# Kernel tuning notes

Hardware: AMD Instinct MI355X
Metric: run time of the kernel (lower is better)

The kernel has to match this reference:

```python
import jax, jax.numpy as jnp
import numpy as np

B, A, N_IN, N_POINTS = 64, 256, 512, 2048


def _sq_cdist(u, v):
    # |u_i - v_j|^2 via expansion, abs() as in the torch original
    d = -2.0 * (u @ v.T) + (u * u).sum(1)[:, None] + (v * v).sum(1)[None, :]
    return jnp.abs(d)


def setup_inputs() -> dict:
    key = jax.random.key(0)
    k1, k2, k3, k4 = jax.random.split(key, 4)
    x = jax.random.normal(k1, (B, A, N_IN), dtype=jnp.float32)
    atom_mask = jax.random.bernoulli(k2, 0.8, (B, A))  # ragged valid-atom mask
    inducing_points = jax.random.normal(k3, (N_POINTS, N_IN), dtype=jnp.float32)
    gamma = (1.0 + 0.25 * jax.random.normal(k4, (N_IN,), dtype=jnp.float32)) * np.sqrt(N_IN).astype(np.float32)
    return {"x": x, "atom_mask": atom_mask, "inducing_points": inducing_points, "gamma": gamma}


def reference(x, atom_mask, inducing_points, gamma):
    b, a, n_in = x.shape
    m = atom_mask.astype(x.dtype)                      # [B, A]
    mf = m[..., None]                                  # [B, A, 1]
    n = m.sum()
    # masked mean / unbiased std over valid atoms (torch .std is ddof=1)
    mean = (x * mf).sum((0, 1)) / n                    # [n_in]
    var = (((x - mean) ** 2) * mf).sum((0, 1)) / (n - 1.0)
    std = jnp.sqrt(var) + 1e-5                         # [n_in]
    xn = (x - mean) / std * mf                         # zero out padded atoms

    g2 = gamma ** 2 + 0.001                            # [n_in]
    z = (xn / g2).reshape(b * a, n_in)                 # [N, n_in]
    zi = inducing_points / g2                          # [M, n_in]

    Kx = jnp.exp(-_sq_cdist(z, zi))                    # [N, M]
    Kind = jnp.exp(-_sq_cdist(zi, zi))                 # [M, M]
    Kinv = jnp.linalg.inv(Kind + 0.05 * jnp.eye(Kind.shape[0], dtype=x.dtype))

    t = Kx @ Kinv                                      # [N, M]
    x_new = ((t @ inducing_points) * std + mean).reshape(b, a, n_in) * mf
    var_out = (1.0 - (t * Kx).sum(-1)).reshape(b, a) * m
    return x_new, var_out
```

## Files before the change

### kernel.cpp

```cpp
#include <hip/hip_runtime.h>
#include <math.h>
#include <stdint.h>

namespace {

constexpr int NROW = 16384;
constexpr int NF   = 512;
constexpr int MIND = 2048;
constexpr float CC = 0.98f;

typedef _Float16 half8 __attribute__((ext_vector_type(8)));
typedef float floatx4 __attribute__((ext_vector_type(4)));

__device__ __forceinline__ void gload16(const void* g, void* l) {
  __builtin_amdgcn_global_load_lds(
      (__attribute__((address_space(1))) void*)g,
      (__attribute__((address_space(3))) void*)l, 16, 0, 0);
}

__global__ __launch_bounds__(256) void stats_kernel(
    const float* __restrict__ x, const int* __restrict__ mask,
    float* __restrict__ sum, float* __restrict__ sumsq, float* __restrict__ cnt)
{
  const int t = threadIdx.x;
  const int row0 = blockIdx.x * 64;
  float s0 = 0.f, s1 = 0.f, q0 = 0.f, q1 = 0.f, c = 0.f;
  for (int r = 0; r < 64; ++r) {
    const int row = row0 + r;
    const float m = (mask[row] != 0) ? 1.f : 0.f;
    const float v0 = x[(size_t)row * NF + t];
    const float v1 = x[(size_t)row * NF + t + 256];
    s0 += m * v0; q0 += m * v0 * v0;
    s1 += m * v1; q1 += m * v1 * v1;
    c += m;
  }
  atomicAdd(&sum[t], s0);        atomicAdd(&sum[t + 256], s1);
  atomicAdd(&sumsq[t], q0);      atomicAdd(&sumsq[t + 256], q1);
  if (t == 0) atomicAdd(cnt, c);
}

__global__ __launch_bounds__(256) void finalize_stats(
    const float* __restrict__ sum, const float* __restrict__ sumsq,
    const float* __restrict__ cnt, const float* __restrict__ gamma,
    float* __restrict__ meanv, float* __restrict__ stdv,
    float* __restrict__ zsv, float* __restrict__ giv)
{
  const int f = blockIdx.x * 256 + threadIdx.x;
  const float n = cnt[0];
  const float mu = sum[f] / n;
  const float var = (sumsq[f] - sum[f] * mu) / (n - 1.0f);
  const float sd = sqrtf(var) + 1e-5f;
  const float g = gamma[f];
  const float g2 = g * g + 0.001f;
  meanv[f] = mu;
  stdv[f]  = sd;
  zsv[f]   = 1.0f / (sd * g2);
  giv[f]   = 1.0f / g2;
}

__global__ __launch_bounds__(256) void make_z(
    const float* __restrict__ x, const int* __restrict__ mask,
    const float* __restrict__ ip, const float* __restrict__ meanv,
    const float* __restrict__ zsv, const float* __restrict__ giv,
    _Float16* __restrict__ Zh, _Float16* __restrict__ Zih,
    float* __restrict__ rnorm, float* __restrict__ cnorm)
{
  const int row = blockIdx.x;
  const int t = threadIdx.x;
  float v0, v1;
  if (row < NROW) {
    const float m = (mask[row] != 0) ? 1.f : 0.f;
    v0 = (x[(size_t)row * NF + t      ] - meanv[t      ]) * zsv[t      ] * m;
    v1 = (x[(size_t)row * NF + t + 256] - meanv[t + 256]) * zsv[t + 256] * m;
    const _Float16 h0 = (_Float16)v0, h1 = (_Float16)v1;
    Zh[(size_t)row * NF + t] = h0;
    Zh[(size_t)row * NF + t + 256] = h1;
    v0 = (float)h0; v1 = (float)h1;
  } else {
    const int r = row - NROW;
    v0 = ip[(size_t)r * NF + t      ] * giv[t      ];
    v1 = ip[(size_t)r * NF + t + 256] * giv[t + 256];
    const _Float16 h0 = (_Float16)v0, h1 = (_Float16)v1;
    Zih[(size_t)r * NF + t] = h0;
    Zih[(size_t)r * NF + t + 256] = h1;
    v0 = (float)h0; v1 = (float)h1;
  }
  float nrm = v0 * v0 + v1 * v1;
  #pragma unroll
  for (int off = 32; off; off >>= 1) nrm += __shfl_xor(nrm, off);
  __shared__ float red[4];
  if ((t & 63) == 0) red[t >> 6] = nrm;
  __syncthreads();
  if (t == 0) {
    const float s = red[0] + red[1] + red[2] + red[3];
    if (row < NROW) rnorm[row] = s; else cnorm[row - NROW] = s;
  }
}

template <int EPI>
__global__ __launch_bounds__(256) void mfma_gemm(
    const _Float16* __restrict__ A, const _Float16* __restrict__ B,
    int M, int N, int K,
    const float* __restrict__ rn, const float* __restrict__ cn,
    _Float16* __restrict__ DKout, float* __restrict__ Cf,
    const _Float16* __restrict__ DK, const float* __restrict__ u,
    float* __restrict__ varacc,
    const float* __restrict__ colsumR,
    const float* __restrict__ stdv, const float* __restrict__ meanv,
    const int* __restrict__ mask)
{
  __shared__ __align__(16) _Float16 As[128 * 32];
  __shared__ __align__(16) _Float16 Bs[128 * 32];
  const int tid = threadIdx.x;
  const int w = tid >> 6, L = tid & 63;
  const int wm = w >> 1, wn = w & 1;
  const int bn = blockIdx.x, bm = blockIdx.y;
  const int lq = L >> 4;
  const int lr = L & 15;

  floatx4 acc[4][4] = {};

  const _Float16* Ag = A + (size_t)(bm * 128) * K;
  const _Float16* Bg = B + (size_t)(bn * 128) * K;
  const int srow = w * 32 + (L >> 2);
  const int scol = (L & 3) * 8;

  for (int k0 = 0; k0 < K; k0 += 32) {
    #pragma unroll
    for (int t = 0; t < 2; ++t) {
      const int r = srow + t * 16;
      gload16(Ag + (size_t)r * K + k0 + scol, As + r * 32 + scol);
      gload16(Bg + (size_t)r * K + k0 + scol, Bs + r * 32 + scol);
    }
    __syncthreads();
    half8 af[4], bf[4];
    #pragma unroll
    for (int mi = 0; mi < 4; ++mi)
      af[mi] = *(const half8*)&As[(wm * 64 + mi * 16 + lr) * 32 + lq * 8];
    #pragma unroll
    for (int ni = 0; ni < 4; ++ni)
      bf[ni] = *(const half8*)&Bs[(wn * 64 + ni * 16 + lr) * 32 + lq * 8];
    #pragma unroll
    for (int mi = 0; mi < 4; ++mi)
      #pragma unroll
      for (int ni = 0; ni < 4; ++ni)
        acc[mi][ni] = __builtin_amdgcn_mfma_f32_16x16x32_f16(
            af[mi], bf[ni], acc[mi][ni], 0, 0, 0);
    __syncthreads();
  }

  const int grb = bm * 128 + wm * 64;
  const int gcb = bn * 128 + wn * 64;

  if constexpr (EPI == 2) {
    #pragma unroll
    for (int mi = 0; mi < 4; ++mi)
      #pragma unroll
      for (int e = 0; e < 4; ++e) {
        const int gr = grb + mi * 16 + lq * 4 + e;
        float partial = 0.f;
        #pragma unroll
        for (int ni = 0; ni < 4; ++ni) {
          const int gc = gcb + ni * 16 + lr;
          const float t = acc[mi][ni][e] + CC * u[gc];
          const float kx = CC + (float)DK[(size_t)gr * N + gc];
          partial += t * kx;
        }
        partial += __shfl_xor(partial, 1);
        partial += __shfl_xor(partial, 2);
        partial += __shfl_xor(partial, 4);
        partial += __shfl_xor(partial, 8);
        if (lr == 0) atomicAdd(&varacc[gr], partial);
      }
  } else if constexpr (EPI == 3) {
    #pragma unroll
    for (int mi = 0; mi < 4; ++mi)
      #pragma unroll
      for (int e = 0; e < 4; ++e) {
        const int gr = grb + mi * 16 + lq * 4 + e;
        const float mrow = (mask[gr] != 0) ? 1.f : 0.f;
        #pragma unroll
        for (int ni = 0; ni < 4; ++ni) {
          const int gc = gcb + ni * 16 + lr;
          const float v = acc[mi][ni][e] + CC * colsumR[gc];
          Cf[(size_t)gr * N + gc] = (v * stdv[gc] + meanv[gc]) * mrow;
        }
      }
  } else {
    #pragma unroll
    for (int mi = 0; mi < 4; ++mi)
      #pragma unroll
      for (int e = 0; e < 4; ++e) {
        const int gr = grb + mi * 16 + lq * 4 + e;
        const float rni = rn[gr];
        #pragma unroll
        for (int ni = 0; ni < 4; ++ni) {
          const int gc = gcb + ni * 16 + lr;
          const float d = rni + cn[gc] - 2.f * acc[mi][ni][e];
          float kx = expf(-fabsf(d));
          if constexpr (EPI == 0) {
            DKout[(size_t)gr * N + gc] = (_Float16)(kx - CC);
          } else {
            if (gr == gc) kx += 0.05f;
            Cf[(size_t)gr * N + gc] = kx;
          }
        }
      }
  }
}

__global__ __launch_bounds__(256) void gemm_f32(
    const float* __restrict__ A, const float* __restrict__ B,
    float* __restrict__ C, int M, int N, int K)
{
  constexpr int BM = 64, BN = 64, BK = 16;
  const int tid = threadIdx.x;
  const int tx = tid % 16, ty = tid / 16;
  const int bn = blockIdx.x, bm = blockIdx.y;
  __shared__ float As[BK][BM + 4];
  __shared__ float Bs[BK][BN + 4];
  float acc[4][4] = {};
  const float* Ag = A + (size_t)bm * BM * K;
  const float* Bg = B + bn * BN;
  for (int k0 = 0; k0 < K; k0 += BK) {
    {
      const int r = tid >> 2, c4 = (tid & 3) << 2;
      const float4 av = *(const float4*)(Ag + (size_t)r * K + k0 + c4);
      As[c4 + 0][r] = av.x; As[c4 + 1][r] = av.y;
      As[c4 + 2][r] = av.z; As[c4 + 3][r] = av.w;
      const int kr = tid / 16, nc = (tid % 16) << 2;
      *(float4*)&Bs[kr][nc] = *(const float4*)(Bg + (size_t)(k0 + kr) * N + nc);
    }
    __syncthreads();
    #pragma unroll
    for (int kk = 0; kk < BK; ++kk) {
      const float4 a4 = *(const float4*)&As[kk][ty * 4];
      const float4 b4 = *(const float4*)&Bs[kk][tx * 4];
      const float a[4] = {a4.x, a4.y, a4.z, a4.w};
      const float b[4] = {b4.x, b4.y, b4.z, b4.w};
      #pragma unroll
      for (int i = 0; i < 4; ++i)
        #pragma unroll
        for (int j = 0; j < 4; ++j) acc[i][j] += a[i] * b[j];
    }
    __syncthreads();
  }
  #pragma unroll
  for (int i = 0; i < 4; ++i) {
    float4 o4; o4.x = acc[i][0]; o4.y = acc[i][1]; o4.z = acc[i][2]; o4.w = acc[i][3];
    *(float4*)(C + (size_t)(bm * BM + ty * 4 + i) * N + bn * BN + tx * 4) = o4;
  }
}


__global__ __launch_bounds__(256) void gj_diag(
    float* __restrict__ A, float* __restrict__ Pall, int k)
{
  const int o = k * 64;
  __shared__ float D[64][68];
  const int t = threadIdx.x;
  #pragma unroll
  for (int l = 0; l < 4; ++l) {
    const int v = t + l * 256;
    const int r = v >> 4, c4 = (v & 15) << 2;
    *(float4*)&D[r][c4] = *(const float4*)(A + (size_t)(o + r) * MIND + o + c4);
  }
  __syncthreads();
  const int i = t >> 2, c0 = (t & 3) * 16;
  for (int s = 0; s < 64; ++s) {
    const float p = 1.0f / D[s][s];
    if (t < 64 && t != s) D[s][t] *= p;
    __syncthreads();
    if (i != s) {
      const float f = D[i][s];
      #pragma unroll
      for (int c = c0; c < c0 + 16; c += 4) {
        float4 ds = *(const float4*)&D[s][c];
        float4 di = *(const float4*)&D[i][c];
        di.x -= f * ds.x; di.y -= f * ds.y; di.z -= f * ds.z; di.w -= f * ds.w;
        *(float4*)&D[i][c] = di;
      }
      if (s >= c0 && s < c0 + 16) D[i][s] = -f * p;
    }
    if (t == 0) D[s][s] = p;
    __syncthreads();
  }
  float* P = Pall + k * 4096;
  #pragma unroll
  for (int l = 0; l < 4; ++l) {
    const int v = t + l * 256;
    const int r = v >> 4, c4 = (v & 15) << 2;
    const float4 dv = *(const float4*)&D[r][c4];
    *(float4*)(P + r * 64 + c4) = dv;
    *(float4*)(A + (size_t)(o + r) * MIND + o + c4) = dv;
  }
}

__global__ __launch_bounds__(256) void gj_prep(
    const float* __restrict__ A, const float* __restrict__ Pall,
    float* __restrict__ CP, float* __restrict__ Bsave, int k)
{
  const int o = k * 64;
  const int t = threadIdx.x;
  if (blockIdx.x >= 32) {
    const int j0 = (blockIdx.x - 32) * 64;
    #pragma unroll
    for (int l = 0; l < 4; ++l) {
      const int v = t + l * 256;
      const int r = v >> 4, c4 = (v & 15) << 2;
      *(float4*)(Bsave + r * MIND + j0 + c4) =
          *(const float4*)(A + (size_t)(o + r) * MIND + j0 + c4);
    }
    return;
  }
  const int i0 = blockIdx.x * 64;
  if (i0 == o) return;
  const float* P = Pall + k * 4096;
  __shared__ float At[64][68];
  __shared__ float Pl[64][68];
  #pragma unroll
  for (int l = 0; l < 4; ++l) {
    const int v = t + l * 256;
    const int r = v >> 4, c4 = (v & 15) << 2;
    const float4 av = *(const float4*)(A + (size_t)(i0 + r) * MIND + o + c4);
    At[c4 + 0][r] = av.x; At[c4 + 1][r] = av.y;
    At[c4 + 2][r] = av.z; At[c4 + 3][r] = av.w;
    *(float4*)&Pl[r][c4] = *(const float4*)(P + r * 64 + c4);
  }
  __syncthreads();
  const int ty = t >> 4, tx = t & 15;
  float acc[4][4] = {};
  for (int s = 0; s < 64; ++s) {
    const float4 a4 = *(const float4*)&At[s][ty * 4];
    const float4 b4 = *(const float4*)&Pl[s][tx * 4];
    const float a[4] = {a4.x, a4.y, a4.z, a4.w};
    const float b[4] = {b4.x, b4.y, b4.z, b4.w};
    #pragma unroll
    for (int i = 0; i < 4; ++i)
      #pragma unroll
      for (int j = 0; j < 4; ++j) acc[i][j] += a[i] * b[j];
  }
  #pragma unroll
  for (int i = 0; i < 4; ++i) {
    float4 o4; o4.x = acc[i][0]; o4.y = acc[i][1]; o4.z = acc[i][2]; o4.w = acc[i][3];
    *(float4*)(CP + (i0 + ty * 4 + i) * 64 + tx * 4) = o4;
  }
}

__global__ __launch_bounds__(256) void gj_apply(
    float* __restrict__ A, float* __restrict__ Pall,
    const float* __restrict__ CP, const float* __restrict__ Bsave, int k)
{
  const int o = k * 64;
  const int i0 = blockIdx.y * 64, j0 = blockIdx.x * 64;
  const int t = threadIdx.x;

  if (i0 == o && j0 == o) return;

  if (j0 == o) {
    #pragma unroll
    for (int l = 0; l < 4; ++l) {
      const int v = t + l * 256;
      const int r = v >> 4, c4 = (v & 15) << 2;
      float4 x = *(const float4*)(CP + (i0 + r) * 64 + c4);
      x.x = -x.x; x.y = -x.y; x.z = -x.z; x.w = -x.w;
      *(float4*)(A + (size_t)(i0 + r) * MIND + o + c4) = x;
    }
    return;
  }

  __shared__ float S1[64 * 68];
  __shared__ float S2[64 * 68];
  #define DD(r, c) S1[(r) * 68 + (c)]

  const bool isrow = (i0 == o);
  const float* Lsrc = isrow ? (Pall + k * 4096) : (CP + i0 * 64);
  #pragma unroll
  for (int l = 0; l < 4; ++l) {
    const int v = t + l * 256;
    const int r = v >> 4, c4 = (v & 15) << 2;
    const float4 lv = *(const float4*)(Lsrc + r * 64 + c4);
    S1[(c4 + 0) * 68 + r] = lv.x; S1[(c4 + 1) * 68 + r] = lv.y;
    S1[(c4 + 2) * 68 + r] = lv.z; S1[(c4 + 3) * 68 + r] = lv.w;
    *(float4*)&S2[r * 68 + c4] = *(const float4*)(Bsave + r * MIND + j0 + c4);
  }
  __syncthreads();
  const int ty = t >> 4, tx = t & 15;
  float acc[4][4] = {};
  for (int s = 0; s < 64; ++s) {
    const float4 a4 = *(const float4*)&S1[s * 68 + ty * 4];
    const float4 b4 = *(const float4*)&S2[s * 68 + tx * 4];
    const float a[4] = {a4.x, a4.y, a4.z, a4.w};
    const float b[4] = {b4.x, b4.y, b4.z, b4.w};
    #pragma unroll
    for (int i = 0; i < 4; ++i)
      #pragma unroll
      for (int j = 0; j < 4; ++j) acc[i][j] += a[i] * b[j];
  }

  if (isrow) {
    #pragma unroll
    for (int i = 0; i < 4; ++i) {
      float4 o4; o4.x = acc[i][0]; o4.y = acc[i][1]; o4.z = acc[i][2]; o4.w = acc[i][3];
      *(float4*)(A + (size_t)(o + ty * 4 + i) * MIND + j0 + tx * 4) = o4;
    }
    return;
  }

  const bool isdiagnext = (i0 == o + 64) && (j0 == o + 64);
  if (!isdiagnext) {
    #pragma unroll
    for (int i = 0; i < 4; ++i) {
      float* cp = A + (size_t)(i0 + ty * 4 + i) * MIND + j0 + tx * 4;
      float4 cv = *(const float4*)cp;
      cv.x -= acc[i][0]; cv.y -= acc[i][1]; cv.z -= acc[i][2]; cv.w -= acc[i][3];
      *(float4*)cp = cv;
    }
    return;
  }

  __syncthreads();
  #pragma unroll
  for (int i = 0; i < 4; ++i) {
    const float4 cv = *(const float4*)(A + (size_t)(i0 + ty * 4 + i) * MIND + j0 + tx * 4);
    DD(ty * 4 + i, tx * 4 + 0) = cv.x - acc[i][0];
    DD(ty * 4 + i, tx * 4 + 1) = cv.y - acc[i][1];
    DD(ty * 4 + i, tx * 4 + 2) = cv.z - acc[i][2];
    DD(ty * 4 + i, tx * 4 + 3) = cv.w - acc[i][3];
  }
  __syncthreads();
  const int di = t >> 2, c0 = (t & 3) * 16;
  for (int s = 0; s < 64; ++s) {
    const float p = 1.0f / DD(s, s);
    if (t < 64 && t != s) DD(s, t) *= p;
    __syncthreads();
    if (di != s) {
      const float f = DD(di, s);
      #pragma unroll
      for (int c = c0; c < c0 + 16; c += 4) {
        float4 ds = *(const float4*)&DD(s, c);
        float4 dv = *(const float4*)&DD(di, c);
        dv.x -= f * ds.x; dv.y -= f * ds.y; dv.z -= f * ds.z; dv.w -= f * ds.w;
        *(float4*)&DD(di, c) = dv;
      }
      if (s >= c0 && s < c0 + 16) DD(di, s) = -f * p;
    }
    if (t == 0) DD(s, s) = p;
    __syncthreads();
  }
  float* Pn = Pall + (k + 1) * 4096;
  #pragma unroll
  for (int l = 0; l < 4; ++l) {
    const int v = t + l * 256;
    const int r = v >> 4, c4 = (v & 15) << 2;
    const float4 dv = *(const float4*)&DD(r, c4);
    *(float4*)(Pn + r * 64 + c4) = dv;
    *(float4*)(A + (size_t)(i0 + r) * MIND + j0 + c4) = dv;
  }
  #undef DD
}

__global__ __launch_bounds__(256) void rowsum_kernel(
    const float* __restrict__ Ai, float* __restrict__ u)
{
  const int row = blockIdx.x * 4 + (threadIdx.x >> 6);
  const int lane = threadIdx.x & 63;
  float s = 0.f;
  for (int c = lane; c < MIND; c += 64) s += Ai[(size_t)row * MIND + c];
  #pragma unroll
  for (int off = 32; off; off >>= 1) s += __shfl_xor(s, off);
  if (lane == 0) u[row] = s;
}

typedef _Float16 half4v __attribute__((ext_vector_type(4)));
__global__ __launch_bounds__(256) void cast_half4(
    const float* __restrict__ s, _Float16* __restrict__ d)
{
  const int i = (blockIdx.x * 256 + threadIdx.x) * 4;
  const float4 v = *(const float4*)(s + i);
  half4v h; h.x = (_Float16)v.x; h.y = (_Float16)v.y;
  h.z = (_Float16)v.z; h.w = (_Float16)v.w;
  *(half4v*)(d + i) = h;
}

__global__ __launch_bounds__(256) void transpose_cast(
    const float* __restrict__ R, _Float16* __restrict__ Rt)
{
  __shared__ float T[64][65];
  const int j0 = blockIdx.x * 64;
  const int f0 = blockIdx.y * 64;
  const int t = threadIdx.x;
  #pragma unroll
  for (int l = 0; l < 16; ++l) {
    const int idx = t + l * 256;
    T[idx >> 6][idx & 63] = R[(size_t)(j0 + (idx >> 6)) * NF + f0 + (idx & 63)];
  }
  __syncthreads();
  #pragma unroll
  for (int l = 0; l < 16; ++l) {
    const int idx = t + l * 256;
    const int fr = idx >> 6, jc = idx & 63;
    Rt[(size_t)(f0 + fr) * MIND + j0 + jc] = (_Float16)T[jc][fr];
  }
}

__global__ __launch_bounds__(256) void colsum_kernel(
    const float* __restrict__ R, float* __restrict__ cs)
{
  const int b = blockIdx.x;
  const int t = threadIdx.x;
  float s0 = 0.f, s1 = 0.f;
  for (int r = 0; r < 64; ++r) {
    s0 += R[(size_t)(b * 64 + r) * NF + t];
    s1 += R[(size_t)(b * 64 + r) * NF + t + 256];
  }
  atomicAdd(&cs[t], s0); atomicAdd(&cs[t + 256], s1);
}

__global__ __launch_bounds__(256) void var_finalize(
    const float* __restrict__ varacc, const int* __restrict__ mask,
    float* __restrict__ outv)
{
  const int i = blockIdx.x * 256 + threadIdx.x;
  const float m = (mask[i] != 0) ? 1.f : 0.f;
  outv[i] = (1.0f - varacc[i]) * m;
}

}

extern "C" void kernel_launch(void* const* d_in, const int* in_sizes, int n_in,
                              void* d_out, int out_size, void* d_ws, size_t ws_size,
                              hipStream_t stream)
{
  (void)in_sizes; (void)n_in; (void)out_size; (void)ws_size;
  const float* x     = (const float*)d_in[0];
  const int*   mask  = (const int*)d_in[1];
  const float* ip    = (const float*)d_in[2];
  const float* gamma = (const float*)d_in[3];
  float* out = (float*)d_out;

  float* w       = (float*)d_ws;
  float* sum     = w;
  float* sumsq   = w + 512;
  float* cnt     = w + 1024;
  float* varacc  = w + 1536;
  float* colsumR = w + 17920;
  float* meanv   = w + 18432;
  float* stdv    = w + 18944;
  float* zsv     = w + 19456;
  float* giv     = w + 19968;
  float* rnorm   = w + 20480;
  float* cnorm   = w + 36864;
  float* u       = w + 38912;
  float* Ai      = w + 40960;
  float* R       = w + 4235264;
  float* Pall    = w + 5283840;
  float* CP      = w + 5414912;
  float* Bsave   = w + 5545984;
  _Float16* hb   = (_Float16*)(w + 5677056);
  _Float16* Zh   = hb;
  _Float16* Zih  = hb + 8388608;
  _Float16* DK   = hb + 9437184;
  _Float16* Kih  = hb + 42991616;
  _Float16* Rt   = hb + 47185920;

  hipMemsetAsync(w, 0, 18432 * sizeof(float), stream);

  stats_kernel<<<256, 256, 0, stream>>>(x, mask, sum, sumsq, cnt);
  finalize_stats<<<2, 256, 0, stream>>>(sum, sumsq, cnt, gamma, meanv, stdv, zsv, giv);
  make_z<<<NROW + MIND, 256, 0, stream>>>(x, mask, ip, meanv, zsv, giv, Zh, Zih, rnorm, cnorm);

  mfma_gemm<0><<<dim3(MIND / 128, NROW / 128), 256, 0, stream>>>(
      Zh, Zih, NROW, MIND, NF, rnorm, cnorm,
      DK, nullptr, nullptr, nullptr, nullptr, nullptr, nullptr, nullptr, nullptr);
  mfma_gemm<1><<<dim3(MIND / 128, MIND / 128), 256, 0, stream>>>(
      Zih, Zih, MIND, MIND, NF, cnorm, cnorm,
      nullptr, Ai, nullptr, nullptr, nullptr, nullptr, nullptr, nullptr, nullptr);

  gj_diag<<<1, 256, 0, stream>>>(Ai, Pall, 0);
  gj_prep<<<64, 256, 0, stream>>>(Ai, Pall, CP, Bsave, 0);
  for (int k = 0; k < 32; ++k) {
    gj_apply<<<dim3(32, 32), 256, 0, stream>>>(Ai, Pall, CP, Bsave, k);
    if (k < 31) gj_prep<<<64, 256, 0, stream>>>(Ai, Pall, CP, Bsave, k + 1);
  }

  gemm_f32<<<dim3(NF / 64, MIND / 64), 256, 0, stream>>>(Ai, ip, R, MIND, NF, MIND);
  transpose_cast<<<dim3(MIND / 64, NF / 64), 256, 0, stream>>>(R, Rt);
  colsum_kernel<<<MIND / 64, 256, 0, stream>>>(R, colsumR);
  rowsum_kernel<<<MIND / 4, 256, 0, stream>>>(Ai, u);
  cast_half4<<<(MIND * MIND) / 1024, 256, 0, stream>>>(Ai, Kih);

  mfma_gemm<2><<<dim3(MIND / 128, NROW / 128), 256, 0, stream>>>(
      DK, Kih, NROW, MIND, MIND, nullptr, nullptr,
      nullptr, nullptr, DK, u, varacc, nullptr, nullptr, nullptr, nullptr);

  mfma_gemm<3><<<dim3(NF / 128, NROW / 128), 256, 0, stream>>>(
      DK, Rt, NROW, NF, MIND, nullptr, nullptr,
      nullptr, out, nullptr, nullptr, nullptr, colsumR, stdv, meanv, mask);

  var_finalize<<<NROW / 256, 256, 0, stream>>>(varacc, mask, out + (size_t)NROW * NF);
}
```

Baseline: 2.170 ms.

## Add 256x256 multi-stage pipelined MFMA GEMM for the two large GEMMs

Introduces a 512-thread GEMM kernel with 256x256 block tiles and a 4-deep LDS ring buffer filled by direct global-to-LDS loads. Staging is gated with manual vmcnt waits and barriers, LDS reads are XOR-swizzled, and MFMA sections run at raised wave priority. It replaces the 128x128 kernel for the distance/exp GEMM and the Kx@Kinv variance GEMM. The goal is to hide load latency, increase data reuse and cut LDS bank conflicts. In exchange it uses 128 KB of LDS and many accumulator registers per block, and fewer blocks fit at once.

```diff
diff --git a/kernel.cpp b/kernel.cpp
--- a/kernel.cpp
+++ b/kernel.cpp
@@ -17,6 +17,9 @@
       (__attribute__((address_space(1))) void*)g,
       (__attribute__((address_space(3))) void*)l, 16, 0, 0);
 }
+
+#define MEMFENCE asm volatile("" ::: "memory")
+#define GATE(N) asm volatile("s_waitcnt vmcnt(" #N ")" ::: "memory")
 
 __global__ __launch_bounds__(256) void stats_kernel(
     const float* __restrict__ x, const int* __restrict__ mask,
@@ -98,6 +101,141 @@
 }
 
 template <int EPI>
+__global__ __launch_bounds__(512, 2) void mfma_gemm256(
+    const _Float16* __restrict__ A, const _Float16* __restrict__ B,
+    int M, int N, int K,
+    const float* __restrict__ rn, const float* __restrict__ cn,
+    _Float16* __restrict__ DKout,
+    const _Float16* __restrict__ DK, const float* __restrict__ u,
+    float* __restrict__ varacc)
+{
+  __shared__ __align__(16) _Float16 Asmem[4][256 * 32];
+  __shared__ __align__(16) _Float16 Bsmem[4][256 * 32];
+
+  const int tid = threadIdx.x;
+  const int w = tid >> 6, L = tid & 63;
+  const int wm = w >> 2, wn = w & 3;
+  const int lq = L >> 4, lr = L & 15;
+  const int bn = blockIdx.x, bm = blockIdx.y;
+  const int NT = K >> 5;
+
+  const int srow  = tid >> 2;
+  const int sslot = tid & 3;
+  const int gslot = sslot ^ ((tid >> 3) & 3);
+  const _Float16* Ag = A + (size_t)(bm * 256 + srow) * K + gslot * 8;
+  const _Float16* Bg = B + (size_t)(bn * 256 + srow) * K + gslot * 8;
+  const size_t rstride = (size_t)128 * K;
+  const int ldst = srow * 32 + sslot * 8;
+
+  const int fswz = (lq ^ ((lr >> 1) & 3)) * 8;
+  const int aoff = (wm * 128 + lr) * 32 + fswz;
+  const int boff = (wn * 64  + lr) * 32 + fswz;
+
+  floatx4 acc[8][4] = {};
+
+  auto stageA = [&](int t) {
+    _Float16* dst = Asmem[t & 3] + ldst;
+    const _Float16* src = Ag + (size_t)t * 32;
+    gload16(src, dst);
+    gload16(src + rstride, dst + 128 * 32);
+  };
+  auto stageB = [&](int t) {
+    _Float16* dst = Bsmem[t & 3] + ldst;
+    const _Float16* src = Bg + (size_t)t * 32;
+    gload16(src, dst);
+    gload16(src + rstride, dst + 128 * 32);
+  };
+
+  stageA(0); stageB(0);
+  if (NT > 1) { stageA(1); stageB(1); }
+  if (NT > 2) { stageA(2); stageB(2); }
+  if (NT > 2)      { GATE(8); }
+  else if (NT > 1) { GATE(4); }
+  else             { GATE(0); }
+  __builtin_amdgcn_s_barrier();
+  MEMFENCE;
+
+  for (int t = 0; t < NT; ++t) {
+    const _Float16* As = Asmem[t & 3];
+    const _Float16* Bs = Bsmem[t & 3];
+    half8 af[4], bf[4], af2[4];
+
+    #pragma unroll
+    for (int mi = 0; mi < 4; ++mi) af[mi] = *(const half8*)&As[aoff + mi * 512];
+    #pragma unroll
+    for (int ni = 0; ni < 4; ++ni) bf[ni] = *(const half8*)&Bs[boff + ni * 512];
+    if (t + 3 < NT) stageA(t + 3);
+    MEMFENCE;
+    __builtin_amdgcn_s_barrier();
+    MEMFENCE;
+    __builtin_amdgcn_s_setprio(1);
+    #pragma unroll
+    for (int mi = 0; mi < 4; ++mi)
+      #pragma unroll
+      for (int ni = 0; ni < 4; ++ni)
+        acc[mi][ni] = __builtin_amdgcn_mfma_f32_16x16x32_f16(
+            af[mi], bf[ni], acc[mi][ni], 0, 0, 0);
+    __builtin_amdgcn_s_setprio(0);
+
+    #pragma unroll
+    for (int mi = 0; mi < 4; ++mi)
+      af2[mi] = *(const half8*)&As[aoff + (mi + 4) * 512];
+    if (t + 3 < NT) stageB(t + 3);
+    if (t + 4 <= NT)      { GATE(8); }
+    else if (t + 3 == NT) { GATE(4); }
+    else if (t + 2 == NT) { GATE(0); }
+    __builtin_amdgcn_s_barrier();
+    MEMFENCE;
+    __builtin_amdgcn_s_setprio(1);
+    #pragma unroll
+    for (int mi = 0; mi < 4; ++mi)
+      #pragma unroll
+      for (int ni = 0; ni < 4; ++ni)
+        acc[mi + 4][ni] = __builtin_amdgcn_mfma_f32_16x16x32_f16(
+            af2[mi], bf[ni], acc[mi + 4][ni], 0, 0, 0);
+    __builtin_amdgcn_s_setprio(0);
+  }
+
+  const int grb = bm * 256 + wm * 128;
+  const int gcb = bn * 256 + wn * 64;
+
+  if constexpr (EPI == 0) {
+    #pragma unroll
+    for (int mi = 0; mi < 8; ++mi)
+      #pragma unroll
+      for (int e = 0; e < 4; ++e) {
+        const int gr = grb + mi * 16 + lq * 4 + e;
+        const float rni = rn[gr];
+        #pragma unroll
+        for (int ni = 0; ni < 4; ++ni) {
+          const int gc = gcb + ni * 16 + lr;
+          const float d = rni + cn[gc] - 2.f * acc[mi][ni][e];
+          DKout[(size_t)gr * N + gc] = (_Float16)(expf(-fabsf(d)) - CC);
+        }
+      }
+  } else {
+    #pragma unroll
+    for (int mi = 0; mi < 8; ++mi)
+      #pragma unroll
+      for (int e = 0; e < 4; ++e) {
+        const int gr = grb + mi * 16 + lq * 4 + e;
+        float partial = 0.f;
+        #pragma unroll
+        for (int ni = 0; ni < 4; ++ni) {
+          const int gc = gcb + ni * 16 + lr;
+          const float tv = acc[mi][ni][e] + CC * u[gc];
+          partial += tv * (CC + (float)DK[(size_t)gr * N + gc]);
+        }
+        partial += __shfl_xor(partial, 1);
+        partial += __shfl_xor(partial, 2);
+        partial += __shfl_xor(partial, 4);
+        partial += __shfl_xor(partial, 8);
+        if (lr == 0) atomicAdd(&varacc[gr], partial);
+      }
+  }
+}
+
+template <int EPI>
 __global__ __launch_bounds__(256) void mfma_gemm(
     const _Float16* __restrict__ A, const _Float16* __restrict__ B,
     int M, int N, int K,
@@ -152,27 +290,7 @@
   const int grb = bm * 128 + wm * 64;
   const int gcb = bn * 128 + wn * 64;
 
-  if constexpr (EPI == 2) {
-    #pragma unroll
-    for (int mi = 0; mi < 4; ++mi)
-      #pragma unroll
-      for (int e = 0; e < 4; ++e) {
-        const int gr = grb + mi * 16 + lq * 4 + e;
-        float partial = 0.f;
-        #pragma unroll
-        for (int ni = 0; ni < 4; ++ni) {
-          const int gc = gcb + ni * 16 + lr;
-          const float t = acc[mi][ni][e] + CC * u[gc];
-          const float kx = CC + (float)DK[(size_t)gr * N + gc];
-          partial += t * kx;
-        }
-        partial += __shfl_xor(partial, 1);
-        partial += __shfl_xor(partial, 2);
-        partial += __shfl_xor(partial, 4);
-        partial += __shfl_xor(partial, 8);
-        if (lr == 0) atomicAdd(&varacc[gr], partial);
-      }
-  } else if constexpr (EPI == 3) {
+  if constexpr (EPI == 3) {
     #pragma unroll
     for (int mi = 0; mi < 4; ++mi)
       #pragma unroll
@@ -198,12 +316,8 @@
           const int gc = gcb + ni * 16 + lr;
           const float d = rni + cn[gc] - 2.f * acc[mi][ni][e];
           float kx = expf(-fabsf(d));
-          if constexpr (EPI == 0) {
-            DKout[(size_t)gr * N + gc] = (_Float16)(kx - CC);
-          } else {
-            if (gr == gc) kx += 0.05f;
-            Cf[(size_t)gr * N + gc] = kx;
-          }
+          if (gr == gc) kx += 0.05f;
+          Cf[(size_t)gr * N + gc] = kx;
         }
       }
   }
@@ -570,9 +684,9 @@
   finalize_stats<<<2, 256, 0, stream>>>(sum, sumsq, cnt, gamma, meanv, stdv, zsv, giv);
   make_z<<<NROW + MIND, 256, 0, stream>>>(x, mask, ip, meanv, zsv, giv, Zh, Zih, rnorm, cnorm);
 
-  mfma_gemm<0><<<dim3(MIND / 128, NROW / 128), 256, 0, stream>>>(
+  mfma_gemm256<0><<<dim3(MIND / 256, NROW / 256), 512, 0, stream>>>(
       Zh, Zih, NROW, MIND, NF, rnorm, cnorm,
-      DK, nullptr, nullptr, nullptr, nullptr, nullptr, nullptr, nullptr, nullptr);
+      DK, nullptr, nullptr, nullptr);
   mfma_gemm<1><<<dim3(MIND / 128, MIND / 128), 256, 0, stream>>>(
       Zih, Zih, MIND, MIND, NF, cnorm, cnorm,
       nullptr, Ai, nullptr, nullptr, nullptr, nullptr, nullptr, nullptr, nullptr);
@@ -590,9 +704,9 @@
   rowsum_kernel<<<MIND / 4, 256, 0, stream>>>(Ai, u);
   cast_half4<<<(MIND * MIND) / 1024, 256, 0, stream>>>(Ai, Kih);
 
-  mfma_gemm<2><<<dim3(MIND / 128, NROW / 128), 256, 0, stream>>>(
+  mfma_gemm256<2><<<dim3(MIND / 256, NROW / 256), 512, 0, stream>>>(
       DK, Kih, NROW, MIND, MIND, nullptr, nullptr,
-      nullptr, nullptr, DK, u, varacc, nullptr, nullptr, nullptr, nullptr);
+      nullptr, DK, u, varacc);
 
   mfma_gemm<3><<<dim3(NF / 128, NROW / 128), 256, 0, stream>>>(
       DK, Rt, NROW, NF, MIND, nullptr, nullptr,
```

Measured after the change: 2.110 ms. 2.8% less time.
